# Performance work log

Hardware: AMD Instinct MI355X
Metric: run time of the kernel (lower is better)

The kernel has to match this reference:

```python
import jax, jax.numpy as jnp
import numpy as np

B = 512
M = 50
N = 50
G = 1            # args.g
ITER = 4         # args.iter_50
EPS = 1e-8


def image2matrix_vit(x):
    # x: [b,1,28,28] -> [b,49,16] (4x4 non-overlapping patches, row-major)
    b = x.shape[0]
    t = x[:, 0].reshape(b, 7, 4, 7, 4)
    return t.transpose(0, 1, 3, 2, 4).reshape(b, 49, 16)


def maxpool2d(x, kh, kw, sh, sw):
    # x: [b,1,H,W], VALID max pooling (matches F.max_pool2d)
    return jax.lax.reduce_window(x, -jnp.inf, jax.lax.max,
                                 (1, 1, kh, kw), (1, 1, sh, sw), 'VALID')


def optical_mvm(inp, w, full_sig):
    # inp: [b,50,50] normalized input, w: [b,50,50] normalized weight (pre-transpose)
    w = jnp.swapaxes(w, 1, 2)
    indim1 = inp.shape[1]       # 50
    odim2 = w.shape[1]          # 50
    out_row = inp.shape[-2]     # 50
    A = jnp.repeat(jnp.repeat(inp, G, axis=1), ITER, axis=2)   # [b,50,200]
    Bm = jnp.repeat(jnp.repeat(w, G, axis=1), ITER, axis=2)    # [b,50,200]
    pr = (4 * M - A.shape[-2]) // 2
    pc = (4 * N - A.shape[-1]) // 2
    A = jnp.pad(A, ((0, 0), (pr, pr), (pc, pc)))               # [b,200,200]
    Bm = jnp.pad(Bm, ((0, 0), (pr, pr), (pc, pc)))
    # precomputed reference spectrum (args.fft_sig_50)
    fft_sig = jnp.fft.fftshift(jnp.fft.fft(full_sig, axis=0), axes=0)
    fft_full = jnp.fft.fftshift(jnp.fft.fft(full_sig[None] * A, axis=1), axes=1)
    opc = fft_full * Bm
    opc_fft = jnp.abs(jnp.fft.fftshift(jnp.fft.fft(opc, axis=2), axes=2))
    r0, r1 = 2 * M - odim2, 2 * M + odim2          # 50:150
    c0, c1 = 2 * N + N // indim1, 3 * N + 3        # 101:153
    temp = opc_fft[:, r0:r1, c0:c1][:, None]       # [b,1,100,52]
    Cmat = maxpool2d(temp, 2, 3, 2, N // indim1)   # [b,1,50,50]
    amp = jnp.abs(fft_sig)[r0:r1, c0:c1][None, None]
    amp = maxpool2d(amp, 2, 3, 2, N // indim1)     # [1,1,50,50]
    amp = amp / (jnp.max(amp) + EPS)
    res = jnp.abs(Cmat / amp)[:, 0]                # [b,50,50]
    res = res / (jnp.max(res, axis=(1, 2), keepdims=True) + EPS)
    return jnp.swapaxes(res, 1, 2)[:, :out_row, :odim2]


def matrix_multiply_optical(inp, w, full_sig):
    # inp: [b,50,50]; w: [50,50] (already abs+padded)
    b = inp.shape[0]
    wb = jnp.broadcast_to(w.T[None], (b,) + w.T.shape)       # [b,50,50]
    imax = jnp.max(inp, axis=-1, keepdims=True)              # [b,50,1]
    inpn = inp / (imax + EPS)
    wmax = jnp.max(wb, axis=-2, keepdims=True)               # [b,1,50]
    wn = wb / (wmax + EPS)
    max_multi = imax @ wmax                                  # [b,50,50]
    out = optical_mvm(inpn, wn, full_sig).astype(jnp.float32)
    return out * max_multi


def setup_inputs() -> dict:
    key = jax.random.key(0)
    k1, k2, k3, k4 = jax.random.split(key, 4)
    inp = jax.random.uniform(k1, (B, 1, 28, 28), dtype=jnp.float32)
    weight = jax.random.normal(k2, (50, 16), dtype=jnp.float32) * 0.1
    bias = jax.random.normal(k3, (1, 49, 50), dtype=jnp.float32) * 0.01
    full_sig = jax.random.uniform(k4, (4 * M, 4 * N), dtype=jnp.float32)
    return {"input": inp, "weight": weight, "bias": bias, "full_sig": full_sig}


def reference(input, weight, bias, full_sig):
    x = image2matrix_vit(input)                  # [b,49,16]
    w = jnp.abs(weight)                          # exp_type != 'standard_mmm'
    out1 = x.shape[1]                            # 49
    x = jnp.pad(x, ((0, 0), (0, 50 - x.shape[1]), (0, 50 - x.shape[2])))
    w = jnp.pad(w, ((0, 50 - w.shape[0]), (0, 50 - w.shape[1])))
    out = matrix_multiply_optical(x, w, full_sig)
    return out[:, :out1, :50] + bias             # bias broadcasts over batch
```

## Files before the change

kernel.cpp:

```cpp
#include <hip/hip_runtime.h>
#include <math.h>

#define EPS 1e-8f
#define TWOPI 6.2831853071795864769f

typedef _Float16 h8 __attribute__((ext_vector_type(8)));
typedef float f32x16 __attribute__((ext_vector_type(16)));

#define WS_WMAX 0
#define WS_WN   64
#define WS_RCPA 1024
#define WS_A2   8192
#define WS_B3   16384


__global__ __launch_bounds__(256) void k_prelude(const float* __restrict__ w,
                                                 const float* __restrict__ fs,
                                                 float* __restrict__ ws) {
    const int blk = blockIdx.x, t = threadIdx.x;
    if (blk < 163) {
        __shared__ float tc[200], tsn[200];
        for (int i = t; i < 200; i += 256) {
            float s, c;
            sincosf(-TWOPI * (float)i / 200.f, &s, &c);
            tc[i] = c; tsn[i] = s;
        }
        __syncthreads();
        int gid = blk * 256 + t;
        int q = gid >> 3, part = gid & 7;
        float aR = 0.f, aI = 0.f;
        if (q < 5200) {
            int s_ = q / 52, u = q - s_ * 52;
            int k = (150 + s_) % 200;
            int j = 101 + u;
            int ph = (k * (part * 25)) % 200;
            for (int r = part * 25; r < part * 25 + 25; ++r) {
                float v = fs[r * 200 + j];
                aR = fmaf(v, tc[ph], aR);
                aI = fmaf(v, tsn[ph], aI);
                ph += k; if (ph >= 200) ph -= 200;
            }
        }
        aR += __shfl_xor(aR, 1); aI += __shfl_xor(aI, 1);
        aR += __shfl_xor(aR, 2); aI += __shfl_xor(aI, 2);
        aR += __shfl_xor(aR, 4); aI += __shfl_xor(aI, 4);
        if (q < 5200 && part == 0)
            ws[WS_RCPA + q] = 1.0f / sqrtf(aR * aR + aI * aI);
    } else {
        int gid = (blk - 163) * 256 + t;
        if (gid < 50) {
            float mx = 0.f, vals[16];
            for (int q = 0; q < 16; ++q) {
                float v = fabsf(w[gid * 16 + q]);
                vals[q] = v; mx = fmaxf(mx, v);
            }
            ws[WS_WMAX + gid] = mx;
            float d = mx + EPS;
            for (int q = 0; q < 16; ++q) ws[WS_WN + gid * 16 + q] = vals[q] / d;
        }
        {
            _Float16* A2h = (_Float16*)(ws + WS_A2);
            int a = gid;
            int s = a & 7, l = (a >> 3) & 63, pks = (a >> 9) & 3, tm = a >> 11;
            int row = 32 * tm + (l & 31);
            int k = 16 * pks + 8 * (l >> 5) + s;
            float X = 0.f;
            if (row < 100 && k < 49) {
                int m = (row < 50) ? row : row - 50;
                int kk = (175 + m) % 200;
                int ph = (kk * (75 + k)) % 200;
                float sn, cs;
                sincosf(-TWOPI * (float)ph / 200.f, &sn, &cs);
                X = (row < 50) ? cs : sn;
            }
            A2h[a] = (_Float16)X;
        }
        _Float16* B3h = (_Float16*)(ws + WS_B3);
        for (int bI = gid; bI < 32768; bI += 8192) {
            int s = bI & 7, l = (bI >> 3) & 63, pks = (bI >> 9) & 15, tn = bI >> 13;
            int part = pks >> 3;
            int np = 32 * tn + (l & 31);
            int kap = 16 * (pks & 7) + 8 * (l >> 5) + s;
            float X = 0.f;
            if (np < 104) {
                int cc = np >> 1;
                int j = kap & 63;
                int ph = ((cc + 1) * j) % 200;
                float sn, cs;
                sincosf(-TWOPI * (float)ph / 200.f, &sn, &cs);
                X = (np & 1) ? ((kap < 64) ? sn : cs) : ((kap < 64) ? cs : -sn);
            }
            _Float16 hi = (_Float16)X;
            B3h[bI] = part ? (_Float16)(X - (float)hi) : hi;
        }
    }
}

__global__ __launch_bounds__(512, 6) void k_main(const float* __restrict__ in,
                                                 const float* __restrict__ bias,
                                                 const float* __restrict__ fs,
                                                 const float* __restrict__ ws,
                                                 float* __restrict__ out) {
    __shared__ __align__(16) char R1[16384];
    __shared__ __align__(16) char R2[16640];
    __shared__ float xpat[50][16];
    __shared__ float imax_s[50];
    __shared__ float inv_s[50];
    __shared__ float res_s[26][50];
    __shared__ __align__(16) float red8[8];

    const int t = threadIdx.x;
    const int b = blockIdx.x;
    const int lane = t & 63;
    const int wid = t >> 6;
    const int swid = __builtin_amdgcn_readfirstlane(wid);
    const float* ib = in + b * 784;

    const int p1_l = t & 63;
    const int p1_ksq = (t >> 6) & 3;
    const int p1_tn = t >> 8;
    const int p1_j = (p1_l & 31) + 32 * p1_tn;
    const int p1_i0 = 16 * p1_ksq + 8 * (p1_l >> 5);
    float fsv[8];
    #pragma unroll
    for (int s = 0; s < 8; ++s) {
        int i = p1_i0 + s;
        fsv[s] = (i < 49) ? fs[(75 + i) * 200 + p1_j] : 0.f;
    }

    if (t < 196) {
        int row = t >> 2, s4 = t & 3;
        int pr = row / 7, pc = row - pr * 7;
        float4 v4 = *(const float4*)(ib + (pr * 4 + s4) * 28 + pc * 4);
        *(float4*)(&xpat[row][s4 * 4]) = v4;
        float mx = fmaxf(fmaxf(v4.x, v4.y), fmaxf(v4.z, v4.w));
        mx = fmaxf(mx, __shfl_xor(mx, 1));
        mx = fmaxf(mx, __shfl_xor(mx, 2));
        if (s4 == 0) { imax_s[row] = mx; inv_s[row] = 1.f / (mx + EPS); }
    }
    {
        h8 z;
        #pragma unroll
        for (int s = 0; s < 8; ++s) z[s] = (_Float16)0.f;
        for (int o = t; o < 1040; o += 512) *(h8*)(R2 + (o << 4)) = z;
    }
    __syncthreads();

    {
        h8 hiv, lov;
        #pragma unroll
        for (int s = 0; s < 8; ++s) {
            int i = p1_i0 + s;
            float v = 0.f;
            if (i < 49) v = fsv[s] * xpat[i][p1_j >> 2] * inv_s[i];
            _Float16 hi = (_Float16)v;
            hiv[s] = hi;
            lov[s] = (_Float16)(v - (float)hi);
        }
        _Float16* B2h = (_Float16*)R1;
        const int base0 = ((p1_tn * 8 + p1_ksq) * 64 + p1_l) * 8;
        *(h8*)(B2h + base0) = hiv;
        *(h8*)(B2h + base0 + 2048) = lov;
    }
    __syncthreads();

    {
        const int tm = swid >> 1, tn = swid & 1;
        f32x16 acc0, acc1;
        #pragma unroll
        for (int i = 0; i < 16; ++i) { acc0[i] = 0.f; acc1[i] = 0.f; }
        const h8* wsA2 = (const h8*)(ws + WS_A2);
        #pragma unroll
        for (int kq = 0; kq < 4; ++kq) {
            h8 a   = wsA2[(tm * 4 + kq) * 64 + lane];
            h8 bhi = *(const h8*)(R1 + (((tn * 8 + kq) * 64 + lane) << 4));
            h8 blo = *(const h8*)(R1 + (((tn * 8 + kq + 4) * 64 + lane) << 4));
            acc0 = __builtin_amdgcn_mfma_f32_32x32x16_f16(a, bhi, acc0, 0, 0, 0);
            acc1 = __builtin_amdgcn_mfma_f32_32x32x16_f16(a, blo, acc1, 0, 0, 0);
        }
        f32x16 acc = acc0 + acc1;
        const float* wn = ws + WS_WN;
        const int j = (lane & 31) + 32 * tn;
        const int q = j >> 2;
        _Float16* A3h = (_Float16*)R2;
        #pragma unroll
        for (int r = 0; r < 16; ++r) {
            int row = (r & 3) + 8 * (r >> 2) + 4 * (lane >> 5) + 32 * tm;
            if (row < 100) {
                int m = (row < 50) ? row : row - 50;
                float v = acc[r] * wn[m * 16 + q];
                int kap = j + ((row < 50) ? 0 : 64);
                int tm3 = m >> 5;
                int pks = kap >> 4;
                int bb = (kap >> 3) & 1;
                int elem = ((tm3 * 8 + pks) * 65 + (m & 31) + 33 * bb) * 8 + (kap & 7);
                A3h[elem] = (_Float16)v;
            }
        }
    }
    __syncthreads();

    {
        const int tm3 = swid >> 2, tn3 = swid & 3;
        f32x16 acc0, acc1;
        #pragma unroll
        for (int i = 0; i < 16; ++i) { acc0[i] = 0.f; acc1[i] = 0.f; }
        const h8* wsB3 = (const h8*)(ws + WS_B3);
        const int aoff = lane + (lane >> 5);
        #pragma unroll
        for (int kq = 0; kq < 8; ++kq) {
            h8 a   = *(const h8*)(R2 + (((tm3 * 8 + kq) * 65 + aoff) << 4));
            h8 bhi = wsB3[(tn3 * 16 + kq) * 64 + lane];
            h8 blo = wsB3[(tn3 * 16 + kq + 8) * 64 + lane];
            acc0 = __builtin_amdgcn_mfma_f32_32x32x16_f16(a, bhi, acc0, 0, 0, 0);
            acc1 = __builtin_amdgcn_mfma_f32_32x32x16_f16(a, blo, acc1, 0, 0, 0);
        }
        f32x16 acc = acc0 + acc1;
        const int np = (lane & 31) + 32 * tn3;
        float* aG = (float*)R1;
        if (np < 104) {
            const int cc = np >> 1;
            const bool wr = !(np & 1);
            #pragma unroll
            for (int r = 0; r < 16; ++r) {
                int row = (r & 3) + 8 * (r >> 2) + 4 * (lane >> 5) + 32 * tm3;
                float g = acc[r];
                float gp = __shfl_xor(g, 1);
                if (row < 50 && wr) aG[row * 52 + cc] = sqrtf(g * g + gp * gp);
            }
        }
    }
    __syncthreads();

    const float* ra = ws + WS_RCPA;
    const float* aG = (const float*)R1;
    float local = 0.f;
    for (int o = t; o < 1300; o += 512) {
        int hh = o / 50, w2 = o - hh * 50;
        int h = hh + 12;
        int m1 = 2 * h - 25, m2 = m1 + 1;
        float v = 0.f;
        #pragma unroll
        for (int du = 0; du < 3; ++du) {
            int u = w2 + du;
            if (m1 >= 0) v = fmaxf(v, aG[m1 * 52 + u]);
            if (m2 < 50) v = fmaxf(v, aG[m2 * 52 + u]);
        }
        float rc = ra[(2 * h) * 52 + w2];
        #pragma unroll
        for (int du = 1; du < 3; ++du) rc = fminf(rc, ra[(2 * h) * 52 + w2 + du]);
        #pragma unroll
        for (int du = 0; du < 3; ++du) rc = fminf(rc, ra[(2 * h + 1) * 52 + w2 + du]);
        float r = v * rc;
        res_s[hh][w2] = r;
        local = fmaxf(local, r);
    }
    #pragma unroll
    for (int off = 32; off > 0; off >>= 1)
        local = fmaxf(local, __shfl_xor(local, off));
    if (lane == 0) red8[wid] = local;
    __syncthreads();

    float mres;
    {
        float4 r0 = *(const float4*)&red8[0];
        float4 r1 = *(const float4*)&red8[4];
        float m0 = fmaxf(fmaxf(r0.x, r0.y), fmaxf(r0.z, r0.w));
        float m1 = fmaxf(fmaxf(r1.x, r1.y), fmaxf(r1.z, r1.w));
        mres = fmaxf(m0, m1);
    }
    float invm = 1.f / (mres + EPS);

    const float* wmaxg = ws + WS_WMAX;
    for (int o = t; o < 2450; o += 512) {
        int r = o / 50, c = o - r * 50;
        float val = bias[o];
        if (c >= 12 && c < 38)
            val = fmaf(res_s[c - 12][r] * invm, imax_s[r] * wmaxg[c], val);
        out[b * 2450 + o] = val;
    }
}

extern "C" void kernel_launch(void* const* d_in, const int* in_sizes, int n_in,
                              void* d_out, int out_size, void* d_ws, size_t ws_size,
                              hipStream_t stream) {
    const float* in   = (const float*)d_in[0];
    const float* w    = (const float*)d_in[1];
    const float* bias = (const float*)d_in[2];
    const float* fs   = (const float*)d_in[3];
    float* out = (float*)d_out;
    float* ws  = (float*)d_ws;

    hipLaunchKernelGGL(k_prelude, dim3(195),  dim3(256), 0, stream, w, fs, ws);
    hipLaunchKernelGGL(k_main,    dim3(512),  dim3(512), 0, stream, in, bias, fs, ws, out);
}
```

Before: 24.25 us.

## Prefetch MFMA operands from global into registers early and use hardware sin/cos

Loads the constant A2 and B3 MFMA operand tiles and the normalized-weight values into registers well before the stages that use them, so global-load latency overlaps earlier phases and barriers. The launch bounds occupancy hint drops from 6 to 4 to leave room for the extra registers. Separately, the prelude's sincosf calls become the AMD hardware sin/cos intrinsics, which take the angle in revolutions. This cuts the cost of building the twiddle tables but may lose some accuracy.

New measurement: 26.57 us. 9.6% more time.

```diff
diff --git a/kernel.cpp b/kernel.cpp
--- a/kernel.cpp
+++ b/kernel.cpp
@@ -2,10 +2,15 @@
 #include <math.h>
 
 #define EPS 1e-8f
-#define TWOPI 6.2831853071795864769f
 
 typedef _Float16 h8 __attribute__((ext_vector_type(8)));
 typedef float f32x16 __attribute__((ext_vector_type(16)));
+
+static __device__ __forceinline__ void fsincos(int ph, float* s, float* c) {
+    float x = (float)ph * (-1.0f / 200.0f);
+    *s = __builtin_amdgcn_sinf(x);
+    *c = __builtin_amdgcn_cosf(x);
+}
 
 #define WS_WMAX 0
 #define WS_WN   64
@@ -22,7 +27,7 @@
         __shared__ float tc[200], tsn[200];
         for (int i = t; i < 200; i += 256) {
             float s, c;
-            sincosf(-TWOPI * (float)i / 200.f, &s, &c);
+            fsincos(i, &s, &c);
             tc[i] = c; tsn[i] = s;
         }
         __syncthreads();
@@ -70,7 +75,7 @@
                 int kk = (175 + m) % 200;
                 int ph = (kk * (75 + k)) % 200;
                 float sn, cs;
-                sincosf(-TWOPI * (float)ph / 200.f, &sn, &cs);
+                fsincos(ph, &sn, &cs);
                 X = (row < 50) ? cs : sn;
             }
             A2h[a] = (_Float16)X;
@@ -87,7 +92,7 @@
                 int j = kap & 63;
                 int ph = ((cc + 1) * j) % 200;
                 float sn, cs;
-                sincosf(-TWOPI * (float)ph / 200.f, &sn, &cs);
+                fsincos(ph, &sn, &cs);
                 X = (np & 1) ? ((kap < 64) ? sn : cs) : ((kap < 64) ? cs : -sn);
             }
             _Float16 hi = (_Float16)X;
@@ -96,7 +101,7 @@
     }
 }
 
-__global__ __launch_bounds__(512, 6) void k_main(const float* __restrict__ in,
+__global__ __launch_bounds__(512, 4) void k_main(const float* __restrict__ in,
                                                  const float* __restrict__ bias,
                                                  const float* __restrict__ fs,
                                                  const float* __restrict__ ws,
@@ -116,6 +121,11 @@
     const int swid = __builtin_amdgcn_readfirstlane(wid);
     const float* ib = in + b * 784;
 
+    const int tmP = swid >> 1, tnP = swid & 1;
+    const int tm3 = swid >> 2, tn3 = swid & 3;
+    const h8* wsA2 = (const h8*)(ws + WS_A2);
+    const h8* wsB3 = (const h8*)(ws + WS_B3);
+
     const int p1_l = t & 63;
     const int p1_ksq = (t >> 6) & 3;
     const int p1_tn = t >> 8;
@@ -127,6 +137,9 @@
         int i = p1_i0 + s;
         fsv[s] = (i < 49) ? fs[(75 + i) * 200 + p1_j] : 0.f;
     }
+    h8 a2f[4];
+    #pragma unroll
+    for (int kq = 0; kq < 4; ++kq) a2f[kq] = wsA2[(tmP * 4 + kq) * 64 + lane];
 
     if (t < 196) {
         int row = t >> 2, s4 = t & 3;
@@ -164,36 +177,47 @@
     }
     __syncthreads();
 
-    {
-        const int tm = swid >> 1, tn = swid & 1;
+    h8 b3h[8], b3l[8];
+    {
+        #pragma unroll
+        for (int k = 0; k < 8; ++k) b3h[k] = wsB3[(tn3 * 16 + k) * 64 + lane];
+        const float* wn = ws + WS_WN;
+        const int j = (lane & 31) + 32 * tnP;
+        const int q = j >> 2;
+        float wnv[16];
+        #pragma unroll
+        for (int r = 0; r < 16; ++r) {
+            int row = (r & 3) + 8 * (r >> 2) + 4 * (lane >> 5) + 32 * tmP;
+            int m = (row < 50) ? row : (row < 100 ? row - 50 : 0);
+            wnv[r] = wn[m * 16 + q];
+        }
+
         f32x16 acc0, acc1;
         #pragma unroll
         for (int i = 0; i < 16; ++i) { acc0[i] = 0.f; acc1[i] = 0.f; }
-        const h8* wsA2 = (const h8*)(ws + WS_A2);
         #pragma unroll
         for (int kq = 0; kq < 4; ++kq) {
-            h8 a   = wsA2[(tm * 4 + kq) * 64 + lane];
-            h8 bhi = *(const h8*)(R1 + (((tn * 8 + kq) * 64 + lane) << 4));
-            h8 blo = *(const h8*)(R1 + (((tn * 8 + kq + 4) * 64 + lane) << 4));
-            acc0 = __builtin_amdgcn_mfma_f32_32x32x16_f16(a, bhi, acc0, 0, 0, 0);
-            acc1 = __builtin_amdgcn_mfma_f32_32x32x16_f16(a, blo, acc1, 0, 0, 0);
-        }
+            h8 bhi = *(const h8*)(R1 + (((tnP * 8 + kq) * 64 + lane) << 4));
+            h8 blo = *(const h8*)(R1 + (((tnP * 8 + kq + 4) * 64 + lane) << 4));
+            acc0 = __builtin_amdgcn_mfma_f32_32x32x16_f16(a2f[kq], bhi, acc0, 0, 0, 0);
+            acc1 = __builtin_amdgcn_mfma_f32_32x32x16_f16(a2f[kq], blo, acc1, 0, 0, 0);
+        }
+        #pragma unroll
+        for (int k = 0; k < 8; ++k) b3l[k] = wsB3[(tn3 * 16 + 8 + k) * 64 + lane];
+
         f32x16 acc = acc0 + acc1;
-        const float* wn = ws + WS_WN;
-        const int j = (lane & 31) + 32 * tn;
-        const int q = j >> 2;
         _Float16* A3h = (_Float16*)R2;
         #pragma unroll
         for (int r = 0; r < 16; ++r) {
-            int row = (r & 3) + 8 * (r >> 2) + 4 * (lane >> 5) + 32 * tm;
+            int row = (r & 3) + 8 * (r >> 2) + 4 * (lane >> 5) + 32 * tmP;
             if (row < 100) {
                 int m = (row < 50) ? row : row - 50;
-                float v = acc[r] * wn[m * 16 + q];
+                float v = acc[r] * wnv[r];
                 int kap = j + ((row < 50) ? 0 : 64);
-                int tm3 = m >> 5;
+                int tmw = m >> 5;
                 int pks = kap >> 4;
                 int bb = (kap >> 3) & 1;
-                int elem = ((tm3 * 8 + pks) * 65 + (m & 31) + 33 * bb) * 8 + (kap & 7);
+                int elem = ((tmw * 8 + pks) * 65 + (m & 31) + 33 * bb) * 8 + (kap & 7);
                 A3h[elem] = (_Float16)v;
             }
         }
@@ -201,19 +225,19 @@
     __syncthreads();
 
     {
-        const int tm3 = swid >> 2, tn3 = swid & 3;
         f32x16 acc0, acc1;
         #pragma unroll
         for (int i = 0; i < 16; ++i) { acc0[i] = 0.f; acc1[i] = 0.f; }
-        const h8* wsB3 = (const h8*)(ws + WS_B3);
         const int aoff = lane + (lane >> 5);
         #pragma unroll
         for (int kq = 0; kq < 8; ++kq) {
-            h8 a   = *(const h8*)(R2 + (((tm3 * 8 + kq) * 65 + aoff) << 4));
-            h8 bhi = wsB3[(tn3 * 16 + kq) * 64 + lane];
-            h8 blo = wsB3[(tn3 * 16 + kq + 8) * 64 + lane];
-            acc0 = __builtin_amdgcn_mfma_f32_32x32x16_f16(a, bhi, acc0, 0, 0, 0);
-            acc1 = __builtin_amdgcn_mfma_f32_32x32x16_f16(a, blo, acc1, 0, 0, 0);
+            h8 a = *(const h8*)(R2 + (((tm3 * 8 + kq) * 65 + aoff) << 4));
+            acc0 = __builtin_amdgcn_mfma_f32_32x32x16_f16(a, b3h[kq], acc0, 0, 0, 0);
+        }
+        #pragma unroll
+        for (int kq = 0; kq < 8; ++kq) {
+            h8 a = *(const h8*)(R2 + (((tm3 * 8 + kq) * 65 + aoff) << 4));
+            acc1 = __builtin_amdgcn_mfma_f32_32x32x16_f16(a, b3l[kq], acc1, 0, 0, 0);
         }
         f32x16 acc = acc0 + acc1;
         const int np = (lane & 31) + 32 * tn3;
```
